# Performance work log

Hardware: AMD Instinct MI355X
Metric: run time of the kernel (lower is better)

## Reference

```python
import jax, jax.numpy as jnp
import numpy as np

B, S, L = 32, 512, 16
VOCAB, NUM_CHAR = 100000, 128
GLOVE_DIM, CHAR_EMB, OUT_DIM = 300, 64, 100


def setup_inputs() -> dict:
    key = jax.random.key(0)
    ks = jax.random.split(key, 9)
    word_tokens = jax.random.randint(ks[0], (B, S), 0, VOCAB)
    char_ids = jax.random.randint(ks[1], (B, S, L), 0, NUM_CHAR)
    char_lens = jax.random.randint(ks[2], (B, S), 1, L + 1)  # >=1 char per word
    glove_table = jax.random.normal(ks[3], (VOCAB, GLOVE_DIM), jnp.float32)
    char_table = jax.random.normal(ks[4], (NUM_CHAR, CHAR_EMB), jnp.float32)
    conv_w = jax.random.normal(ks[5], (OUT_DIM, CHAR_EMB), jnp.float32) / np.sqrt(CHAR_EMB)
    conv_b = jax.random.normal(ks[6], (OUT_DIM,), jnp.float32) * 0.01
    lin_w = jax.random.normal(ks[7], (OUT_DIM, OUT_DIM), jnp.float32) / np.sqrt(OUT_DIM)
    lin_b = jax.random.normal(ks[8], (OUT_DIM,), jnp.float32) * 0.01
    return {
        "word_tokens": word_tokens, "char_ids": char_ids, "char_lens": char_lens,
        "glove_table": glove_table, "char_table": char_table,
        "conv_w": conv_w, "conv_b": conv_b, "lin_w": lin_w, "lin_b": lin_b,
    }


def reference(word_tokens, char_ids, char_lens, glove_table, char_table,
              conv_w, conv_b, lin_w, lin_b):
    # glove lookup: [B, S, GLOVE_DIM]
    glove = glove_table[word_tokens]
    # char embedding: [B, S, L, CHAR_EMB]
    ce = char_table[char_ids]
    # Conv1d with kernel_size=1 == per-position linear: [B, S, L, OUT_DIM]
    conv = jnp.einsum('bsle,oe->bslo', ce, conv_w) + conv_b
    # masked mean over the ragged char dimension (original torch.mean over true length)
    mask = (jnp.arange(conv.shape[2])[None, None, :] < char_lens[..., None]).astype(conv.dtype)
    mean = jnp.sum(conv * mask[..., None], axis=2) / char_lens[..., None].astype(conv.dtype)
    # final linear: [B, S, OUT_DIM]
    char_out = mean @ lin_w.T + lin_b
    # concat glove + char features: [B, S, GLOVE_DIM + OUT_DIM]
    return jnp.concatenate([glove, char_out], axis=-1)
```

## Files before the change

kernel.cpp:

```cpp
#include <hip/hip_runtime.h>

#define LW   16
#define GD   300
#define CEM  64
#define OD   100
#define NCH  128
#define NW   (32 * 512)

__global__ __launch_bounds__(128) void precompute_T(
        const float* __restrict__ char_table, const float* __restrict__ conv_w,
        const float* __restrict__ conv_b,     const float* __restrict__ lin_w,
        const float* __restrict__ lin_b,      float* __restrict__ ws) {
    __shared__ float ceS[CEM];
    __shared__ float U[OD];
    const int t  = threadIdx.x;
    const int ch = blockIdx.x;

    if (t < CEM) ceS[t] = char_table[ch * CEM + t];
    __syncthreads();

    if (t < OD) {
        const float* cw = conv_w + t * CEM;
        float a0 = 0.f, a1 = 0.f, a2 = 0.f, a3 = 0.f;
        #pragma unroll
        for (int e = 0; e < CEM; e += 4) {
            a0 = fmaf(cw[e + 0], ceS[e + 0], a0);
            a1 = fmaf(cw[e + 1], ceS[e + 1], a1);
            a2 = fmaf(cw[e + 2], ceS[e + 2], a2);
            a3 = fmaf(cw[e + 3], ceS[e + 3], a3);
        }
        U[t] = (a0 + a1) + (a2 + a3);
    }
    __syncthreads();

    if (t < OD) {
        const float* lw = lin_w + t * OD;
        float a0 = 0.f, a1 = 0.f, a2 = 0.f, a3 = 0.f;
        #pragma unroll 5
        for (int j = 0; j < OD; j += 4) {
            a0 = fmaf(lw[j + 0], U[j + 0], a0);
            a1 = fmaf(lw[j + 1], U[j + 1], a1);
            a2 = fmaf(lw[j + 2], U[j + 2], a2);
            a3 = fmaf(lw[j + 3], U[j + 3], a3);
        }
        ws[ch * OD + t] = (a0 + a1) + (a2 + a3);

        if (ch == 0) {
            float b0 = lin_b[t], b1 = 0.f, b2 = 0.f, b3 = 0.f;
            #pragma unroll 5
            for (int j = 0; j < OD; j += 4) {
                b0 = fmaf(lw[j + 0], conv_b[j + 0], b0);
                b1 = fmaf(lw[j + 1], conv_b[j + 1], b1);
                b2 = fmaf(lw[j + 2], conv_b[j + 2], b2);
                b3 = fmaf(lw[j + 3], conv_b[j + 3], b3);
            }
            ws[NCH * OD + t] = (b0 + b1) + (b2 + b3);
        }
    }
}

__global__ __launch_bounds__(256) void fused_embed(
        const int*   __restrict__ word_tokens,
        const int*   __restrict__ char_ids,
        const int*   __restrict__ char_lens,
        const float* __restrict__ glove,
        const float* __restrict__ ws,
        float*       __restrict__ out) {
    const int wave = threadIdx.x >> 6;
    const int lane = threadIdx.x & 63;
    const int word = blockIdx.x * 4 + wave;

    const int tok = word_tokens[word];
    const int len = char_lens[word];

    const int4* cid4 = (const int4*)(char_ids + (size_t)word * LW);
    const int4 i0 = cid4[0], i1 = cid4[1], i2 = cid4[2], i3 = cid4[3];

    const float4* g4 = (const float4*)(glove + (size_t)tok * GD);
    float4 g0 = g4[lane];
    float4 g1;
    const bool tail = lane < (GD / 4 - 64);
    if (tail) g1 = g4[64 + lane];
    float4* d4 = (float4*)(out + (size_t)word * (GD + OD));
    d4[lane] = g0;
    if (tail) d4[64 + lane] = g1;

    const float cl = ws[NCH * OD + lane];
    const bool hi = lane < (OD - 64);
    const float chv = ws[NCH * OD + 64 + lane];
    float acc0 = 0.f, acc1 = 0.f;

#define CGROUP(iv, base)                                                   \
    {                                                                      \
        const float* t0 = ws + (iv).x * OD;                                \
        const float* t1 = ws + (iv).y * OD;                                \
        const float* t2 = ws + (iv).z * OD;                                \
        const float* t3 = ws + (iv).w * OD;                                \
        float v0 = t0[lane], w0 = t0[64 + lane];                           \
        float v1 = t1[lane], w1 = t1[64 + lane];                           \
        float v2 = t2[lane], w2 = t2[64 + lane];                           \
        float v3 = t3[lane], w3 = t3[64 + lane];                           \
        acc0 += ((base) + 0 < len) ? v0 : 0.f;                             \
        acc1 += ((base) + 0 < len) ? w0 : 0.f;                             \
        acc0 += ((base) + 1 < len) ? v1 : 0.f;                             \
        acc1 += ((base) + 1 < len) ? w1 : 0.f;                             \
        acc0 += ((base) + 2 < len) ? v2 : 0.f;                             \
        acc1 += ((base) + 2 < len) ? w2 : 0.f;                             \
        acc0 += ((base) + 3 < len) ? v3 : 0.f;                             \
        acc1 += ((base) + 3 < len) ? w3 : 0.f;                             \
    }

    CGROUP(i0, 0)
    if (len > 4)  CGROUP(i1, 4)
    if (len > 8)  CGROUP(i2, 8)
    if (len > 12) CGROUP(i3, 12)
#undef CGROUP

    const float inv = 1.f / (float)len;
    float* co = out + (size_t)word * (GD + OD) + GD;
    co[lane] = fmaf(acc0, inv, cl);
    if (hi) co[64 + lane] = fmaf(acc1, inv, chv);
}

extern "C" void kernel_launch(void* const* d_in, const int* in_sizes, int n_in,
                              void* d_out, int out_size, void* d_ws, size_t ws_size,
                              hipStream_t stream) {
    const int*   word_tokens = (const int*)  d_in[0];
    const int*   char_ids    = (const int*)  d_in[1];
    const int*   char_lens   = (const int*)  d_in[2];
    const float* glove       = (const float*)d_in[3];
    const float* char_table  = (const float*)d_in[4];
    const float* conv_w      = (const float*)d_in[5];
    const float* conv_b      = (const float*)d_in[6];
    const float* lin_w       = (const float*)d_in[7];
    const float* lin_b       = (const float*)d_in[8];
    float* out = (float*)d_out;
    float* ws  = (float*)d_ws;

    precompute_T<<<NCH, 128, 0, stream>>>(char_table, conv_w, conv_b, lin_w, lin_b, ws);

    fused_embed<<<NW / 4, 256, 0, stream>>>(
        word_tokens, char_ids, char_lens, glove, ws, out);
}
```

Measured before the change: 22.28 us.

## Pad projected char table rows to 128 floats and gather them as float2

The precomputed per-character projection table now uses a 128-float row stride. This lets each lane gather one aligned float2 per character, with only the first 50 lanes active, instead of two scalar loads. When a group of four characters is fully inside the word length, the masked per-element selects are replaced by a straight sum. The glove row store is moved after the character loads so more loads are in flight together. The precompute kernel also stages conv_w and lin_w in padded shared memory (about 66KB of LDS) instead of reading each weight row from global memory per thread.

```diff
diff --git a/kernel.cpp b/kernel.cpp
--- a/kernel.cpp
+++ b/kernel.cpp
@@ -6,21 +6,28 @@
 #define OD   100
 #define NCH  128
 #define NW   (32 * 512)
+#define TROW 128
 
 __global__ __launch_bounds__(128) void precompute_T(
         const float* __restrict__ char_table, const float* __restrict__ conv_w,
         const float* __restrict__ conv_b,     const float* __restrict__ lin_w,
         const float* __restrict__ lin_b,      float* __restrict__ ws) {
+    __shared__ float cwS[OD * 65];
+    __shared__ float lwS[OD * 101];
     __shared__ float ceS[CEM];
     __shared__ float U[OD];
     const int t  = threadIdx.x;
     const int ch = blockIdx.x;
 
+    for (int n = t; n < OD * CEM; n += 128)
+        cwS[(n >> 6) * 65 + (n & 63)] = conv_w[n];
+    for (int n = t; n < OD * OD; n += 128)
+        lwS[(n / 100) * 101 + (n % 100)] = lin_w[n];
     if (t < CEM) ceS[t] = char_table[ch * CEM + t];
     __syncthreads();
 
     if (t < OD) {
-        const float* cw = conv_w + t * CEM;
+        const float* cw = cwS + t * 65;
         float a0 = 0.f, a1 = 0.f, a2 = 0.f, a3 = 0.f;
         #pragma unroll
         for (int e = 0; e < CEM; e += 4) {
@@ -34,7 +41,7 @@
     __syncthreads();
 
     if (t < OD) {
-        const float* lw = lin_w + t * OD;
+        const float* lw = lwS + t * 101;
         float a0 = 0.f, a1 = 0.f, a2 = 0.f, a3 = 0.f;
         #pragma unroll 5
         for (int j = 0; j < OD; j += 4) {
@@ -43,7 +50,7 @@
             a2 = fmaf(lw[j + 2], U[j + 2], a2);
             a3 = fmaf(lw[j + 3], U[j + 3], a3);
         }
-        ws[ch * OD + t] = (a0 + a1) + (a2 + a3);
+        ws[ch * TROW + t] = (a0 + a1) + (a2 + a3);
 
         if (ch == 0) {
             float b0 = lin_b[t], b1 = 0.f, b2 = 0.f, b3 = 0.f;
@@ -54,7 +61,7 @@
                 b2 = fmaf(lw[j + 2], conv_b[j + 2], b2);
                 b3 = fmaf(lw[j + 3], conv_b[j + 3], b3);
             }
-            ws[NCH * OD + t] = (b0 + b1) + (b2 + b3);
+            ws[NCH * TROW + t] = (b0 + b1) + (b2 + b3);
         }
     }
 }
@@ -81,45 +88,59 @@
     float4 g1;
     const bool tail = lane < (GD / 4 - 64);
     if (tail) g1 = g4[64 + lane];
+
+    const bool act = lane < OD / 2;
+    float2 cb = {0.f, 0.f};
+    if (act) cb = ((const float2*)(ws + NCH * TROW))[lane];
+
+    float2 acc = {0.f, 0.f};
+
+#define TROWP(id) ((const float2*)(ws + ((id) << 7)))
+#define LOADG(iv, a, b, c, d) \
+    float2 a = TROWP((iv).x)[lane], b = TROWP((iv).y)[lane], \
+           c = TROWP((iv).z)[lane], d = TROWP((iv).w)[lane];
+#define ADDF(a, b, c, d) { \
+    acc.x += ((a.x + b.x) + (c.x + d.x)); \
+    acc.y += ((a.y + b.y) + (c.y + d.y)); }
+#define ADDP(base, a, b, c, d) { \
+    acc.x += ((base) + 0 < len) ? a.x : 0.f;  acc.y += ((base) + 0 < len) ? a.y : 0.f; \
+    acc.x += ((base) + 1 < len) ? b.x : 0.f;  acc.y += ((base) + 1 < len) ? b.y : 0.f; \
+    acc.x += ((base) + 2 < len) ? c.x : 0.f;  acc.y += ((base) + 2 < len) ? c.y : 0.f; \
+    acc.x += ((base) + 3 < len) ? d.x : 0.f;  acc.y += ((base) + 3 < len) ? d.y : 0.f; }
+
+    {
+        LOADG(i0, v0, v1, v2, v3)
+        if (len >= 4) ADDF(v0, v1, v2, v3) else ADDP(0, v0, v1, v2, v3)
+    }
+    if (len > 4) {
+        LOADG(i1, v0, v1, v2, v3)
+        if (len >= 8) ADDF(v0, v1, v2, v3) else ADDP(4, v0, v1, v2, v3)
+    }
+    if (len > 8) {
+        LOADG(i2, v0, v1, v2, v3)
+        if (len >= 12) ADDF(v0, v1, v2, v3) else ADDP(8, v0, v1, v2, v3)
+    }
+    if (len > 12) {
+        LOADG(i3, v0, v1, v2, v3)
+        if (len >= 16) ADDF(v0, v1, v2, v3) else ADDP(12, v0, v1, v2, v3)
+    }
+#undef TROWP
+#undef LOADG
+#undef ADDF
+#undef ADDP
+
     float4* d4 = (float4*)(out + (size_t)word * (GD + OD));
     d4[lane] = g0;
     if (tail) d4[64 + lane] = g1;
 
-    const float cl = ws[NCH * OD + lane];
-    const bool hi = lane < (OD - 64);
-    const float chv = ws[NCH * OD + 64 + lane];
-    float acc0 = 0.f, acc1 = 0.f;
-
-#define CGROUP(iv, base)                                                   \
-    {                                                                      \
-        const float* t0 = ws + (iv).x * OD;                                \
-        const float* t1 = ws + (iv).y * OD;                                \
-        const float* t2 = ws + (iv).z * OD;                                \
-        const float* t3 = ws + (iv).w * OD;                                \
-        float v0 = t0[lane], w0 = t0[64 + lane];                           \
-        float v1 = t1[lane], w1 = t1[64 + lane];                           \
-        float v2 = t2[lane], w2 = t2[64 + lane];                           \
-        float v3 = t3[lane], w3 = t3[64 + lane];                           \
-        acc0 += ((base) + 0 < len) ? v0 : 0.f;                             \
-        acc1 += ((base) + 0 < len) ? w0 : 0.f;                             \
-        acc0 += ((base) + 1 < len) ? v1 : 0.f;                             \
-        acc1 += ((base) + 1 < len) ? w1 : 0.f;                             \
-        acc0 += ((base) + 2 < len) ? v2 : 0.f;                             \
-        acc1 += ((base) + 2 < len) ? w2 : 0.f;                             \
-        acc0 += ((base) + 3 < len) ? v3 : 0.f;                             \
-        acc1 += ((base) + 3 < len) ? w3 : 0.f;                             \
+    const float inv = 1.f / (float)len;
+    float2 r;
+    r.x = fmaf(acc.x, inv, cb.x);
+    r.y = fmaf(acc.y, inv, cb.y);
+    if (act) {
+        float2* co2 = (float2*)(out + (size_t)word * (GD + OD) + GD);
+        co2[lane] = r;
     }
-
-    CGROUP(i0, 0)
-    if (len > 4)  CGROUP(i1, 4)
-    if (len > 8)  CGROUP(i2, 8)
-    if (len > 12) CGROUP(i3, 12)
-#undef CGROUP
-
-    const float inv = 1.f / (float)len;
-    float* co = out + (size_t)word * (GD + OD) + GD;
-    co[lane] = fmaf(acc0, inv, cl);
-    if (hi) co[64 + lane] = fmaf(acc1, inv, chv);
 }
 
 extern "C" void kernel_launch(void* const* d_in, const int* in_sizes, int n_in,
```

New measurement: 28.54 us. 1.28x slower.

## Precompute combined lin_w·conv_w matrix then project char table in separate kernel

Applied to the files above, without the earlier changes.

Replaces the single precompute kernel with two kernels. The first forms the fused weight W = lin_w @ conv_w (stored transposed in workspace) along with the bias vector. The second projects each character embedding through W using coalesced float2 loads. Each per-character dot chain shrinks from 64+100 serial FMAs to 64, but an extra kernel launch is added and the per-char work may be dwarfed by the main gather kernel. Falls back to the old path when the workspace is too small.

```diff
diff --git a/kernel.cpp b/kernel.cpp
--- a/kernel.cpp
+++ b/kernel.cpp
@@ -6,6 +6,73 @@
 #define OD   100
 #define NCH  128
 #define NW   (32 * 512)
+
+#define WCOFF  12928
+#define WSNEED 19456
+
+__global__ __launch_bounds__(64) void k_wc(
+        const float* __restrict__ conv_w, const float* __restrict__ conv_b,
+        const float* __restrict__ lin_w,  const float* __restrict__ lin_b,
+        float* __restrict__ ws) {
+    const int e = threadIdx.x;
+    const int o = blockIdx.x;
+    if (o < OD) {
+        const float* lw = lin_w + o * OD;
+        float a0 = 0.f, a1 = 0.f, a2 = 0.f, a3 = 0.f;
+        #pragma unroll 5
+        for (int j = 0; j < OD; j += 4) {
+            a0 = fmaf(lw[j + 0], conv_w[(j + 0) * CEM + e], a0);
+            a1 = fmaf(lw[j + 1], conv_w[(j + 1) * CEM + e], a1);
+            a2 = fmaf(lw[j + 2], conv_w[(j + 2) * CEM + e], a2);
+            a3 = fmaf(lw[j + 3], conv_w[(j + 3) * CEM + e], a3);
+        }
+        ws[WCOFF + e * OD + o] = (a0 + a1) + (a2 + a3);
+    } else {
+        {
+            const float* lw = lin_w + e * OD;
+            float b0 = lin_b[e], b1 = 0.f, b2 = 0.f, b3 = 0.f;
+            #pragma unroll 5
+            for (int j = 0; j < OD; j += 4) {
+                b0 = fmaf(lw[j + 0], conv_b[j + 0], b0);
+                b1 = fmaf(lw[j + 1], conv_b[j + 1], b1);
+                b2 = fmaf(lw[j + 2], conv_b[j + 2], b2);
+                b3 = fmaf(lw[j + 3], conv_b[j + 3], b3);
+            }
+            ws[NCH * OD + e] = (b0 + b1) + (b2 + b3);
+        }
+        if (e < OD - 64) {
+            const float* lw = lin_w + (64 + e) * OD;
+            float b0 = lin_b[64 + e], b1 = 0.f, b2 = 0.f, b3 = 0.f;
+            #pragma unroll 5
+            for (int j = 0; j < OD; j += 4) {
+                b0 = fmaf(lw[j + 0], conv_b[j + 0], b0);
+                b1 = fmaf(lw[j + 1], conv_b[j + 1], b1);
+                b2 = fmaf(lw[j + 2], conv_b[j + 2], b2);
+                b3 = fmaf(lw[j + 3], conv_b[j + 3], b3);
+            }
+            ws[NCH * OD + 64 + e] = (b0 + b1) + (b2 + b3);
+        }
+    }
+}
+
+__global__ __launch_bounds__(64) void k_T(
+        const float* __restrict__ char_table, float* __restrict__ ws) {
+    __shared__ float ceS[CEM];
+    const int l  = threadIdx.x;
+    const int ch = blockIdx.x;
+    ceS[l] = char_table[ch * CEM + l];
+    __syncthreads();
+    float2 acc = {0.f, 0.f};
+    #pragma unroll 8
+    for (int e = 0; e < CEM; ++e) {
+        const float  m = ceS[e];
+        const float2 w = ((const float2*)(ws + WCOFF + e * OD))[l];
+        acc.x = fmaf(m, w.x, acc.x);
+        acc.y = fmaf(m, w.y, acc.y);
+    }
+    if (l < OD / 2)
+        ((float2*)(ws + ch * OD))[l] = acc;
+}
 
 __global__ __launch_bounds__(128) void precompute_T(
         const float* __restrict__ char_table, const float* __restrict__ conv_w,
@@ -137,7 +204,13 @@
     float* out = (float*)d_out;
     float* ws  = (float*)d_ws;
 
-    precompute_T<<<NCH, 128, 0, stream>>>(char_table, conv_w, conv_b, lin_w, lin_b, ws);
+    if (ws_size >= (size_t)WSNEED * sizeof(float)) {
+        k_wc<<<OD + 1, 64, 0, stream>>>(conv_w, conv_b, lin_w, lin_b, ws);
+        k_T <<<NCH,    64, 0, stream>>>(char_table, ws);
+    } else {
+        precompute_T<<<NCH, 128, 0, stream>>>(char_table, conv_w, conv_b,
+                                              lin_w, lin_b, ws);
+    }
 
     fused_embed<<<NW / 4, 256, 0, stream>>>(
         word_tokens, char_ids, char_lens, glove, ws, out);
```

New measurement: 25.49 us. 1.14x slower.
